# Optimization experiments

Measured on AMD Instinct MI355X. Metric: run time of the kernel, lower is better.

Reference implementation:

```python
import jax, jax.numpy as jnp
import numpy as np

N_HEADS = 16
KV_HEADS = 4
HEAD_DIM = 128
D_MODEL = N_HEADS * HEAD_DIM  # 2048
KV_DIM = KV_HEADS * HEAD_DIM  # 512
MAX_POS = 4096
ROPE_THETA = 10000.0
EPS = 1e-5


def _rope_cache(seq_len):
    # QEffMolmoRotaryEmbedding: inv_freq over head_dim, emb = cat(freqs, freqs)
    inv_freq = 1.0 / (ROPE_THETA ** (jnp.arange(0, HEAD_DIM, 2, dtype=jnp.float32) / HEAD_DIM))
    t = jnp.arange(seq_len, dtype=jnp.float32)
    freqs = jnp.outer(t, inv_freq)                      # [S, D/2]
    emb = jnp.concatenate([freqs, freqs], axis=-1)      # [S, D]
    return jnp.cos(emb), jnp.sin(emb)


def _rotate_half(x):
    # x: [B, H, T, D] -> cat(-x2, x1) with halves along last dim
    x1, x2 = jnp.split(x, 2, axis=-1)
    return jnp.concatenate([-x2, x1], axis=-1)


def _rms_norm(x, w):
    var = jnp.mean(jnp.square(x), axis=-1, keepdims=True)
    return (x * jax.lax.rsqrt(var + EPS)) * w


def setup_inputs() -> dict:
    key = jax.random.key(0)
    ks = jax.random.split(key, 8)
    B, T = 1, 2048
    q = jax.random.normal(ks[0], (B, T, D_MODEL), dtype=jnp.float32)
    k = jax.random.normal(ks[1], (B, T, KV_DIM), dtype=jnp.float32)
    v = jax.random.normal(ks[2], (B, T, KV_DIM), dtype=jnp.float32)
    # causal mask: True means masked (torch.where(mask, -10000, scores))
    attention_mask = jnp.triu(jnp.ones((T, T), dtype=bool), k=1)[None, None]  # [1,1,T,T]
    position_ids = jnp.arange(T, dtype=jnp.int32)[None, :]                    # [B,T]
    q_norm_w = jax.random.normal(ks[3], (D_MODEL,), dtype=jnp.float32) * 0.02 + 1.0
    k_norm_w = jax.random.normal(ks[4], (KV_DIM,), dtype=jnp.float32) * 0.02 + 1.0
    w_out = jax.random.normal(ks[5], (D_MODEL, D_MODEL), dtype=jnp.float32) * (D_MODEL ** -0.5)
    return {"q": q, "k": k, "v": v, "attention_mask": attention_mask,
            "position_ids": position_ids, "q_norm_w": q_norm_w,
            "k_norm_w": k_norm_w, "w_out": w_out}


def reference(q, k, v, attention_mask, position_ids, q_norm_w, k_norm_w, w_out):
    B, T, C = q.shape
    # QK-norm on flat projections
    q = _rms_norm(q, q_norm_w)
    k = _rms_norm(k, k_norm_w)
    # split heads: [B, H, T, D]
    q = q.reshape(B, T, N_HEADS, HEAD_DIM).transpose(0, 2, 1, 3)
    k = k.reshape(B, T, KV_HEADS, HEAD_DIM).transpose(0, 2, 1, 3)
    v = v.reshape(B, T, KV_HEADS, HEAD_DIM).transpose(0, 2, 1, 3)
    # RoPE (rotate_half variant)
    cos_c, sin_c = _rope_cache(MAX_POS)
    cos = cos_c[position_ids][:, None]  # [B,1,T,D]
    sin = sin_c[position_ids][:, None]
    q = q * cos + _rotate_half(q) * sin
    k = k * cos + _rotate_half(k) * sin
    # GQA expand
    rep = N_HEADS // KV_HEADS
    k = jnp.repeat(k, rep, axis=1)
    v = jnp.repeat(v, rep, axis=1)
    scale = 1.0 / np.sqrt(HEAD_DIM)
    scores = jnp.einsum('bhqd,bhkd->bhqk', q, k) * scale  # [B,H,T,T]
    scores = jnp.where(attention_mask, jnp.float32(-10000.0), scores)
    attn = jax.nn.softmax(scores.astype(jnp.float32), axis=-1).astype(q.dtype)
    out = jnp.einsum('bhqk,bhkd->bhqd', attn, v)          # [B,H,T,D]
    out = out.transpose(0, 2, 1, 3).reshape(B, T, C)
    return out @ w_out.T
```

## Files before the change

kernel.cpp:

```cpp
#include <hip/hip_runtime.h>
#include <hip/hip_bf16.h>
#include <math.h>

#define T_SEQ 2048
#define NH 16
#define KVH 4
#define HD 128
#define DM 2048
#define KVD 512

typedef short bf16x8 __attribute__((ext_vector_type(8)));
typedef float f32x4 __attribute__((ext_vector_type(4)));
typedef float f32x16 __attribute__((ext_vector_type(16)));
typedef unsigned int uint2v __attribute__((ext_vector_type(2)));

static __device__ __forceinline__ unsigned short f2bf(float f) {
    unsigned int x = __float_as_uint(f);
    x += 0x7fff + ((x >> 16) & 1);
    return (unsigned short)(x >> 16);
}
static __device__ __forceinline__ float bf2f(unsigned short u) {
    return __uint_as_float(((unsigned int)u) << 16);
}

static __device__ __forceinline__ unsigned int cvtpk(float lo, float hi) {
    unsigned int r;
    asm("v_cvt_pk_bf16_f32 %0, %1, %2" : "=v"(r) : "v"(lo), "v"(hi));
    return r;
}

static __device__ __forceinline__ f32x4 mfma16(bf16x8 a, bf16x8 b, f32x4 c) {
    return __builtin_amdgcn_mfma_f32_16x16x32_bf16(a, b, c, 0, 0, 0);
}
static __device__ __forceinline__ f32x16 mfma32(bf16x8 a, bf16x8 b, f32x16 c) {
    return __builtin_amdgcn_mfma_f32_32x32x16_bf16(a, b, c, 0, 0, 0);
}

static __device__ __forceinline__ void gl_lds16(const unsigned short* g, unsigned short* l) {
    __builtin_amdgcn_global_load_lds(
        (const __attribute__((address_space(1))) unsigned int*)g,
        (__attribute__((address_space(3))) unsigned int*)l,
        16, 0, 0);
}


__global__ __launch_bounds__(256) void prep_all(
    const float* __restrict__ q, const float* __restrict__ k,
    const float* __restrict__ qw, const float* __restrict__ kw,
    const int* __restrict__ pos_ids,
    unsigned short* __restrict__ Qb, unsigned short* __restrict__ Ks,
    const float* __restrict__ v, unsigned short* __restrict__ Vs,
    const float* __restrict__ w, unsigned short* __restrict__ Wf) {
    int bid = blockIdx.x;
    int tid = threadIdx.x;
    __shared__ float smem[DM + KVD + 64 + 64 + 8];

    if (bid < 2048) {
        float* qr = smem;
        float* kr = smem + DM;
        float* cosL = smem + DM + KVD;
        float* sinL = cosL + 64;
        float* redq = sinL + 64;
        float* redk = redq + 4;
        int t = bid;
        float qs = 0.f, ks = 0.f;
        {
            const float* qp = q + (size_t)t * DM + tid * 8;
            float4 v0 = *(const float4*)(qp);
            float4 v1 = *(const float4*)(qp + 4);
            float* dst = qr + tid * 8;
            dst[0] = v0.x; dst[1] = v0.y; dst[2] = v0.z; dst[3] = v0.w;
            dst[4] = v1.x; dst[5] = v1.y; dst[6] = v1.z; dst[7] = v1.w;
            qs = v0.x * v0.x + v0.y * v0.y + v0.z * v0.z + v0.w * v0.w +
                 v1.x * v1.x + v1.y * v1.y + v1.z * v1.z + v1.w * v1.w;
            float2 kv = *(const float2*)(k + (size_t)t * KVD + tid * 2);
            kr[tid * 2] = kv.x; kr[tid * 2 + 1] = kv.y;
            ks = kv.x * kv.x + kv.y * kv.y;
        }
        if (tid < 64) {
            float pos = (float)pos_ids[t];
            float inv = powf(10000.0f, -(float)tid * (1.0f / 64.0f));
            float a = pos * inv;
            cosL[tid] = cosf(a);
            sinL[tid] = sinf(a);
        }
        for (int off = 32; off; off >>= 1) {
            qs += __shfl_down(qs, off);
            ks += __shfl_down(ks, off);
        }
        if ((tid & 63) == 0) { redq[tid >> 6] = qs; redk[tid >> 6] = ks; }
        __syncthreads();
        float qinv = rsqrtf((redq[0] + redq[1] + redq[2] + redq[3]) * (1.0f / DM) + 1e-5f);
        float kinv = rsqrtf((redk[0] + redk[1] + redk[2] + redk[3]) * (1.0f / KVD) + 1e-5f);
        {
            int base = tid * 8;
            int h = base >> 7;
            int d = base & 127;
            bool lo = d < 64;
            int i0 = d & 63;
            int pb = lo ? base + 64 : base - 64;
            #pragma unroll
            for (int j = 0; j < 8; ++j) {
                float xv = qr[base + j] * qinv * qw[base + j];
                float pv = qr[pb + j] * qinv * qw[pb + j];
                float c = cosL[i0 + j];
                float s = sinL[i0 + j];
                float o = lo ? (xv * c - pv * s) : (xv * c + pv * s);
                Qb[((size_t)h * T_SEQ + t) * HD + d + j] = f2bf(o);
            }
        }
        {
            int base = tid * 2;
            int kh = base >> 7;
            int d = base & 127;
            bool lo = d < 64;
            int i0 = d & 63;
            int pb = lo ? base + 64 : base - 64;
            int kt = t >> 5, lq = t & 31;
            #pragma unroll
            for (int j = 0; j < 2; ++j) {
                float xv = kr[base + j] * kinv * kw[base + j];
                float pv = kr[pb + j] * kinv * kw[pb + j];
                float c = cosL[i0 + j];
                float s = sinL[i0 + j];
                float o = lo ? (xv * c - pv * s) : (xv * c + pv * s);
                int dj = d + j;
                int sl = dj >> 4, hi2 = (dj >> 3) & 1, jj = dj & 7;
                size_t oi = ((((size_t)(kh * 64 + kt) * 8 + sl) * 2 + hi2) * 32 + lq) * 8 + jj;
                Ks[oi] = f2bf(o);
            }
        }
        return;
    }
    if (bid < 2304) {
        unsigned short* tile = (unsigned short*)smem;
        int vb = bid - 2048;
        int tb = vb & 31;
        int cb = vb >> 5;
        #pragma unroll 4
        for (int rep = 0; rep < 16; ++rep) {
            int e = rep * 256 + tid;
            int r = e >> 6;
            int c = e & 63;
            tile[c * 80 + r] = f2bf(v[(size_t)(tb * 64 + r) * KVD + cb * 64 + c]);
        }
        __syncthreads();
        #pragma unroll
        for (int rep = 0; rep < 2; ++rep) {
            int e = rep * 256 + tid;
            int cc = e >> 3, tg = e & 7;
            int cg = cb * 64 + cc;
            int kh = cg >> 7, crow = cg & 127, db = crow >> 5, lq = crow & 31;
            int t0g = tb * 64 + tg * 8;
            int kt = t0g >> 5, tr = t0g & 31, half = tr >> 4, hi2 = (tr >> 3) & 1;
            size_t o = (((((size_t)(kh * 64 + kt) * 2 + half) * 4 + db) * 2 + hi2) * 32 + lq) * 8;
            *(bf16x8*)(Vs + o) = *(const bf16x8*)(&tile[cc * 80 + tg * 8]);
        }
        return;
    }
    {
        size_t idx = ((size_t)(bid - 2304) * 256 + tid) * 4;
        int row = (int)(idx >> 11);
        int col = (int)(idx & 2047);
        float4 f = *(const float4*)(w + idx);
        ushort4 o;
        o.x = f2bf(f.x); o.y = f2bf(f.y); o.z = f2bf(f.z); o.w = f2bf(f.w);
        int nt = row >> 6, wn2 = (row >> 5) & 1, jb = (row >> 4) & 1, lr = row & 15;
        int kt = col >> 6, ks = (col >> 5) & 1, hi2 = (col >> 3) & 3, jj = col & 7;
        size_t off = (((size_t)(nt * 32 + kt) * 8) + (wn2 * 2 + jb) * 2 + ks) * 512
                   + (lr + 16 * hi2) * 8 + jj;
        *(ushort4*)(Wf + off) = o;
    }
}

#define BEXP 20.0f
#define SCALE2 (0.08838834764831845f * 1.4426950408889634f)

#define STAGE1(B, S, KT)                                                           \
    do {                                                                           \
        const unsigned short* kg_ = Kt_g + (size_t)(KT) * 4096;                    \
        const unsigned short* vg_ = Vt_g + (size_t)(KT) * 4096;                    \
        gl_lds16(kg_ + w * 512 + l * 8,        &kv[B][S][w * 512]);                \
        gl_lds16(kg_ + 2048 + w * 512 + l * 8, &kv[B][S][2048 + w * 512]);         \
        gl_lds16(vg_ + w * 512 + l * 8,        &kv[B][S][4096 + w * 512]);         \
        gl_lds16(vg_ + 2048 + w * 512 + l * 8, &kv[B][S][6144 + w * 512]);         \
    } while (0)

#define TILE_COMPUTE(BUF, SLOT, KT)                                                \
    do {                                                                           \
        const unsigned short* kl = &kv[BUF][SLOT][0] + l * 8;                      \
        const unsigned short* vl = &kv[BUF][SLOT][4096] + l * 8;                   \
        f32x16 sa, sb;                                                             \
        _Pragma("unroll") for (int r = 0; r < 16; ++r) { sa[r] = 0.f; sb[r] = 0.f; } \
        __builtin_amdgcn_s_setprio(1);                                             \
        _Pragma("unroll") for (int x = 0; x < 8; x += 2) {                         \
            bf16x8 k0 = *(const bf16x8*)(kl + x * 512);                            \
            bf16x8 k1 = *(const bf16x8*)(kl + (x + 1) * 512);                      \
            sa = mfma32(k0, qf[x], sa);                                            \
            sb = mfma32(k1, qf[x + 1], sb);                                        \
        }                                                                          \
        __builtin_amdgcn_s_setprio(0);                                             \
        float p_[16];                                                              \
        if ((KT) == nkt - 1) {                                                     \
            int lim = qglob - (KT) * 32;                                           \
            _Pragma("unroll") for (int r = 0; r < 16; ++r) {                       \
                float e_ = __builtin_amdgcn_exp2f((sa[r] + sb[r]) * SCALE2 - BEXP); \
                int off_ = (r & 3) + 8 * (r >> 2) + 4 * hi;                        \
                p_[r] = (off_ <= lim) ? e_ : 0.f;                                  \
                sden4[r & 3] += p_[r];                                             \
            }                                                                      \
        } else {                                                                   \
            _Pragma("unroll") for (int r = 0; r < 16; ++r) {                       \
                p_[r] = __builtin_amdgcn_exp2f((sa[r] + sb[r]) * SCALE2 - BEXP);   \
                sden4[r & 3] += p_[r];                                             \
            }                                                                      \
        }                                                                          \
        __builtin_amdgcn_s_setprio(1);                                             \
        _Pragma("unroll") for (int half = 0; half < 2; ++half) {                   \
            unsigned int a0 = cvtpk(p_[half * 8 + 0], p_[half * 8 + 1]);           \
            unsigned int a1 = cvtpk(p_[half * 8 + 2], p_[half * 8 + 3]);           \
            unsigned int b0 = cvtpk(p_[half * 8 + 4], p_[half * 8 + 5]);           \
            unsigned int b1 = cvtpk(p_[half * 8 + 6], p_[half * 8 + 7]);           \
            uint2v w0 = __builtin_amdgcn_permlane32_swap(a0, b0, false, false);    \
            uint2v w1 = __builtin_amdgcn_permlane32_swap(a1, b1, false, false);    \
            union { unsigned int u[4]; bf16x8 v; } pc;                             \
            pc.u[0] = w0[0]; pc.u[1] = w1[0]; pc.u[2] = w0[1]; pc.u[3] = w1[1];    \
            bf16x8 pf = pc.v;                                                      \
            _Pragma("unroll") for (int db = 0; db < 4; ++db) {                     \
                bf16x8 vf = *(const bf16x8*)(vl + (half * 4 + db) * 512);          \
                oacc[db] = mfma32(vf, pf, oacc[db]);                               \
            }                                                                      \
        }                                                                          \
        __builtin_amdgcn_s_setprio(0);                                             \
    } while (0)

__global__ __launch_bounds__(256) void attn_fwd22(
    const unsigned short* __restrict__ Qb, const unsigned short* __restrict__ Ks,
    const unsigned short* __restrict__ Vs,
    unsigned short* __restrict__ Opart, float* __restrict__ Lpart,
    unsigned short* __restrict__ Xf, int CHUNK) {
    int fid = blockIdx.x;
    int sid = fid >> 2;
    int kh = fid & 3;
    int qrow, seg;
    if (sid < 60)       { qrow = 63 - sid / 3;          seg = sid % 3; }
    else if (sid < 104) { int t2 = sid - 60; qrow = 43 - (t2 >> 1); seg = t2 & 1; }
    else                { qrow = 21 - (sid - 104);      seg = 0; }

    int tid = threadIdx.x;
    int w = tid >> 6, l = tid & 63;
    int h = kh * 4 + w;
    int lq = l & 31, hi = l >> 5;
    int qglob = qrow * 32 + lq;

    int nkt = qrow + 1;
    int t0 = seg * CHUNK;
    int t1 = min(t0 + CHUNK, nkt);
    size_t idx = (size_t)(h * 64 + qrow) * 4 + seg;

    const unsigned short* Qh = Qb + (size_t)h * T_SEQ * HD;
    const unsigned short* Kt_g = Ks + (size_t)kh * 64 * 4096;
    const unsigned short* Vt_g = Vs + (size_t)kh * 64 * 4096;

    __shared__ unsigned short kv[2][2][8192];

    bf16x8 qf[8];
    #pragma unroll
    for (int sl = 0; sl < 8; ++sl)
        qf[sl] = *(const bf16x8*)(Qh + (size_t)qglob * HD + sl * 16 + hi * 8);

    f32x16 oacc[4];
    #pragma unroll
    for (int db = 0; db < 4; ++db)
        #pragma unroll
        for (int r = 0; r < 16; ++r) oacc[db][r] = 0.f;
    f32x4 sden4 = (f32x4){0.f, 0.f, 0.f, 0.f};

    int pairsEnd = t0 + ((t1 - t0) & ~1);
    int kt = t0;
    int cur = 0;
    if (kt < pairsEnd) { STAGE1(0, 0, kt); STAGE1(0, 1, kt + 1); }
    if (kt + 2 < pairsEnd) { STAGE1(1, 0, kt + 2); STAGE1(1, 1, kt + 3); }
    for (; kt < pairsEnd; kt += 2) {
        bool more = (kt + 2 < pairsEnd);
        if (more) asm volatile("s_waitcnt vmcnt(8)" ::: "memory");
        else      asm volatile("s_waitcnt vmcnt(0)" ::: "memory");
        __builtin_amdgcn_s_barrier();
        TILE_COMPUTE(cur, 0, kt);
        TILE_COMPUTE(cur, 1, kt + 1);
        asm volatile("s_waitcnt lgkmcnt(0)" ::: "memory");
        __builtin_amdgcn_s_barrier();
        if (kt + 4 < pairsEnd) { STAGE1(cur, 0, kt + 4); STAGE1(cur, 1, kt + 5); }
        cur ^= 1;
    }
    if (kt < t1) {
        STAGE1(cur, 0, kt);
        asm volatile("s_waitcnt vmcnt(0)" ::: "memory");
        __builtin_amdgcn_s_barrier();
        TILE_COMPUTE(cur, 0, kt);
    }

    float sden = (sden4[0] + sden4[1]) + (sden4[2] + sden4[3]);
    float sden_tot = sden + __shfl_xor(sden, 32);

    if (t0 == 0 && t1 == nkt) {
        float invs = 1.0f / sden_tot;
        int mt = qglob >> 7, wmrow = (qglob >> 6) & 1, ii = (qglob >> 4) & 3, lr = qglob & 15;
        size_t baseA = (((size_t)mt * 32) * 16 + (wmrow * 4 + ii) * 2) * 512 + lr * 8;
        #pragma unroll
        for (int db = 0; db < 4; ++db) {
            size_t bdb = baseA + (size_t)(h * 2 + (db >> 1)) * 8192 + (size_t)(db & 1) * 512;
            #pragma unroll
            for (int r = 0; r < 16; ++r) {
                size_t off = bdb + (r >> 2) * 128 + (r & 3) + 4 * hi;
                Xf[off] = f2bf(oacc[db][r] * invs);
            }
        }
        return;
    }
    if (hi == 0) Lpart[idx * 32 + lq] = sden_tot;
    unsigned short* op = Opart + (idx << 12);
    #pragma unroll
    for (int db = 0; db < 4; ++db) {
        #pragma unroll
        for (int r = 0; r < 16; ++r) {
            int d = db * 32 + (r & 3) + 8 * (r >> 2) + 4 * hi;
            op[d * 32 + lq] = f2bf(oacc[db][r]);
        }
    }
}

__global__ __launch_bounds__(256) void attn_combine(
    const unsigned short* __restrict__ Opart, const float* __restrict__ Lpart,
    unsigned short* __restrict__ Xf, int CHUNK) {
    int qrow = CHUNK + blockIdx.x;
    int h = blockIdx.y;
    int tid = threadIdx.x;
    int nkt = qrow + 1;
    int used = (nkt + CHUNK - 1) / CHUNK;
    int base = (h * 64 + qrow) * 4;
    __shared__ float invden[32];
    if (tid < 32) {
        int q = tid;
        float den = 0.f;
        for (int s = 0; s < used; ++s) den += Lpart[(base + s) * 32 + q];
        invden[q] = 1.0f / den;
    }
    __syncthreads();
    int d = tid >> 1, q0 = (tid & 1) * 16;
    float acc[16];
    #pragma unroll
    for (int j = 0; j < 16; ++j) acc[j] = 0.f;
    for (int s = 0; s < used; ++s) {
        const unsigned short* op = Opart + ((size_t)(base + s) << 12) + d * 32 + q0;
        bf16x8 o0 = *(const bf16x8*)(op);
        bf16x8 o1 = *(const bf16x8*)(op + 8);
        #pragma unroll
        for (int j = 0; j < 8; ++j) {
            acc[j]     += bf2f((unsigned short)o0[j]);
            acc[8 + j] += bf2f((unsigned short)o1[j]);
        }
    }
    __shared__ unsigned short xo[32][136];
    #pragma unroll
    for (int j = 0; j < 16; ++j)
        xo[q0 + j][d] = f2bf(acc[j] * invden[q0 + j]);
    __syncthreads();
    int q = tid >> 3, dc = (tid & 7) * 16;
    bf16x8 v0 = *(const bf16x8*)(&xo[q][dc]);
    bf16x8 v1 = *(const bf16x8*)(&xo[q][dc + 8]);
    int row = qrow * 32 + q;
    int mt = row >> 7, wmrow = (row >> 6) & 1, ii = (row >> 4) & 3, lr = row & 15;
    int kt = h * 2 + (dc >> 6);
    int ks = (dc >> 5) & 1;
    int hi2 = (dc >> 3) & 3;
    size_t off = (((size_t)(mt * 32 + kt) * 16) + (wmrow * 4 + ii) * 2 + ks) * 512
               + (lr + 16 * hi2) * 8;
    *(bf16x8*)(Xf + off) = v0;
    *(bf16x8*)(Xf + off + 128) = v1;
}

__global__ __launch_bounds__(256) void outproj3(
    const unsigned short* __restrict__ Xf, const unsigned short* __restrict__ Wf,
    float* __restrict__ out) {
    __shared__ unsigned short Af[2][8192];
    __shared__ unsigned short Bf[2][4096];
    int tid = threadIdx.x;
    int w = tid >> 6, l = tid & 63;
    int lr = l & 15, lg = l >> 4;
    int wm = w >> 1, wn = w & 1;
    int id = blockIdx.x;
    int wg = (id & 7) * 64 + (id >> 3);
    int s = wg >> 5, wi = wg & 31;
    int mb = (s & 3) * 4 + (wi & 3);
    int nb = (s >> 2) * 8 + (wi >> 2);
    int m0 = mb * 128, n0 = nb * 64;

    const unsigned short* Xt = Xf + ((size_t)mb * 32 * 16) * 512 + l * 8;
    const unsigned short* Wt = Wf + ((size_t)nb * 32 * 8) * 512 + l * 8;

    f32x4 acc[4][2];
    #pragma unroll
    for (int i = 0; i < 4; ++i)
        #pragma unroll
        for (int j = 0; j < 2; ++j) acc[i][j] = (f32x4){0.f, 0.f, 0.f, 0.f};

#define OSTAGE(B, KT)                                                              \
    do {                                                                           \
        const unsigned short* xa = Xt + (size_t)(KT) * 8192;                       \
        const unsigned short* wb_ = Wt + (size_t)(KT) * 4096;                      \
        _Pragma("unroll") for (int u = 0; u < 4; ++u)                              \
            gl_lds16(xa + (w * 4 + u) * 512, &Af[B][(w * 4 + u) * 512]);           \
        _Pragma("unroll") for (int u = 0; u < 2; ++u)                              \
            gl_lds16(wb_ + (w * 2 + u) * 512, &Bf[B][(w * 2 + u) * 512]);          \
    } while (0)

    OSTAGE(0, 0);
    OSTAGE(1, 1);
    int cur = 0;
    for (int t = 0; t < 32; ++t) {
        if (t + 1 < 32) asm volatile("s_waitcnt vmcnt(6)" ::: "memory");
        else            asm volatile("s_waitcnt vmcnt(0)" ::: "memory");
        __builtin_amdgcn_s_barrier();
        __builtin_amdgcn_s_setprio(1);
        #pragma unroll
        for (int ks = 0; ks < 2; ++ks) {
            bf16x8 af[4], bfr[2];
            #pragma unroll
            for (int i = 0; i < 4; ++i)
                af[i] = *(const bf16x8*)(&Af[cur][((wm * 4 + i) * 2 + ks) * 512] + l * 8);
            #pragma unroll
            for (int j = 0; j < 2; ++j)
                bfr[j] = *(const bf16x8*)(&Bf[cur][((wn * 2 + j) * 2 + ks) * 512] + l * 8);
            #pragma unroll
            for (int i = 0; i < 4; ++i)
                #pragma unroll
                for (int j = 0; j < 2; ++j)
                    acc[i][j] = mfma16(af[i], bfr[j], acc[i][j]);
        }
        __builtin_amdgcn_s_setprio(0);
        asm volatile("s_waitcnt lgkmcnt(0)" ::: "memory");
        __builtin_amdgcn_s_barrier();
        if (t + 2 < 32) OSTAGE(cur, t + 2);
        cur ^= 1;
    }
    #pragma unroll
    for (int i = 0; i < 4; ++i) {
        #pragma unroll
        for (int j = 0; j < 2; ++j) {
            #pragma unroll
            for (int r = 0; r < 4; ++r) {
                int row = m0 + wm * 64 + i * 16 + lg * 4 + r;
                int col = n0 + wn * 32 + j * 16 + lr;
                out[(size_t)row * DM + col] = acc[i][j][r];
            }
        }
    }
}

extern "C" void kernel_launch(void* const* d_in, const int* in_sizes, int n_in,
                              void* d_out, int out_size, void* d_ws, size_t ws_size,
                              hipStream_t stream) {
    const float* q = (const float*)d_in[0];
    const float* k = (const float*)d_in[1];
    const float* v = (const float*)d_in[2];
    const int* pos_ids = (const int*)d_in[4];
    const float* qw = (const float*)d_in[5];
    const float* kw = (const float*)d_in[6];
    const float* wout = (const float*)d_in[7];
    float* out = (float*)d_out;

    char* ws = (char*)d_ws;
    unsigned short* Qb = (unsigned short*)(ws + 0x100000);
    unsigned short* Ks = (unsigned short*)(ws + 0x900000);
    unsigned short* Vs = (unsigned short*)(ws + 0xB00000);
    unsigned short* Wf = (unsigned short*)(ws + 0xD00000);
    unsigned short* Xf = (unsigned short*)(ws + 0x1500000);
    float* Lpart = (float*)(ws + 0x1D00000);
    unsigned short* Opart = (unsigned short*)(ws + 0x1E00000);

    int CHUNK = (ws_size >= 0x1E00000ull + 4ull * 0x800000ull) ? 22 : 64;

    prep_all<<<2048 + 256 + 4096, 256, 0, stream>>>(q, k, qw, kw, pos_ids, Qb, Ks,
                                                    v, Vs, wout, Wf);
    if (CHUNK == 22) {
        attn_fwd22<<<504, 256, 0, stream>>>(Qb, Ks, Vs, Opart, Lpart, Xf, CHUNK);
        attn_combine<<<dim3(64 - 22, NH), 256, 0, stream>>>(Opart, Lpart, Xf, CHUNK);
    } else {
        attn_fwd22<<<504, 256, 0, stream>>>(Qb, Ks, Vs, Opart, Lpart, Xf, 64);
    }
    outproj3<<<512, 256, 0, stream>>>(Xf, Wf, out);
}
```

Baseline: 85.23 us.

## Enlarge output-projection tile to 128x128 with 512-thread blocks

The output projection GEMM now uses 128x128 output tiles computed by 8 waves in a 512-thread block, instead of 128x64 tiles with 4 waves. Grid size halves to 256 blocks, and the block-to-tile mapping and LDS staging of the weight tile are rearranged so each wave loads two A and two B subtiles. The aim is to raise reuse of the activation tile and cut global/L2 traffic per FLOP. The cost is twice the LDS per block and fewer blocks than CUs on a 256-CU part, which may reduce occupancy and latency hiding.

```diff
diff --git a/kernel.cpp b/kernel.cpp
--- a/kernel.cpp
+++ b/kernel.cpp
@@ -380,24 +380,26 @@
     *(bf16x8*)(Xf + off + 128) = v1;
 }
 
-__global__ __launch_bounds__(256) void outproj3(
+__global__ __launch_bounds__(512) void outproj4(
     const unsigned short* __restrict__ Xf, const unsigned short* __restrict__ Wf,
     float* __restrict__ out) {
     __shared__ unsigned short Af[2][8192];
-    __shared__ unsigned short Bf[2][4096];
+    __shared__ unsigned short Bf[2][8192];
     int tid = threadIdx.x;
     int w = tid >> 6, l = tid & 63;
     int lr = l & 15, lg = l >> 4;
-    int wm = w >> 1, wn = w & 1;
+    int wm = w >> 2, wn = w & 3;
     int id = blockIdx.x;
-    int wg = (id & 7) * 64 + (id >> 3);
-    int s = wg >> 5, wi = wg & 31;
-    int mb = (s & 3) * 4 + (wi & 3);
-    int nb = (s >> 2) * 8 + (wi >> 2);
-    int m0 = mb * 128, n0 = nb * 64;
+    int wg = (id & 7) * 32 + (id >> 3);
+    int mb = wg >> 4, nb = wg & 15;
+    int m0 = mb * 128, n0 = nb * 128;
 
     const unsigned short* Xt = Xf + ((size_t)mb * 32 * 16) * 512 + l * 8;
-    const unsigned short* Wt = Wf + ((size_t)nb * 32 * 8) * 512 + l * 8;
+    const unsigned short* Wp = Wf + ((size_t)(nb * 2 + (w >> 2)) * 32 * 8) * 512 + l * 8;
+    int aw = w * 2;
+    int bw = (w & 3) * 2;
+    unsigned short* BfBase0 = &Bf[0][(w >> 2) * 4096];
+    unsigned short* BfBase1 = &Bf[1][(w >> 2) * 4096];
 
     f32x4 acc[4][2];
     #pragma unroll
@@ -405,21 +407,22 @@
         #pragma unroll
         for (int j = 0; j < 2; ++j) acc[i][j] = (f32x4){0.f, 0.f, 0.f, 0.f};
 
-#define OSTAGE(B, KT)                                                              \
+#define OSTG(B, KT)                                                                \
     do {                                                                           \
         const unsigned short* xa = Xt + (size_t)(KT) * 8192;                       \
-        const unsigned short* wb_ = Wt + (size_t)(KT) * 4096;                      \
-        _Pragma("unroll") for (int u = 0; u < 4; ++u)                              \
-            gl_lds16(xa + (w * 4 + u) * 512, &Af[B][(w * 4 + u) * 512]);           \
-        _Pragma("unroll") for (int u = 0; u < 2; ++u)                              \
-            gl_lds16(wb_ + (w * 2 + u) * 512, &Bf[B][(w * 2 + u) * 512]);          \
+        const unsigned short* wa = Wp + (size_t)(KT) * 4096;                       \
+        gl_lds16(xa + aw * 512,       &Af[B][aw * 512]);                           \
+        gl_lds16(xa + (aw + 1) * 512, &Af[B][(aw + 1) * 512]);                     \
+        unsigned short* bb = (B) ? BfBase1 : BfBase0;                              \
+        gl_lds16(wa + bw * 512,       bb + bw * 512);                              \
+        gl_lds16(wa + (bw + 1) * 512, bb + (bw + 1) * 512);                        \
     } while (0)
 
-    OSTAGE(0, 0);
-    OSTAGE(1, 1);
+    OSTG(0, 0);
+    OSTG(1, 1);
     int cur = 0;
     for (int t = 0; t < 32; ++t) {
-        if (t + 1 < 32) asm volatile("s_waitcnt vmcnt(6)" ::: "memory");
+        if (t + 1 < 32) asm volatile("s_waitcnt vmcnt(4)" ::: "memory");
         else            asm volatile("s_waitcnt vmcnt(0)" ::: "memory");
         __builtin_amdgcn_s_barrier();
         __builtin_amdgcn_s_setprio(1);
@@ -431,7 +434,8 @@
                 af[i] = *(const bf16x8*)(&Af[cur][((wm * 4 + i) * 2 + ks) * 512] + l * 8);
             #pragma unroll
             for (int j = 0; j < 2; ++j)
-                bfr[j] = *(const bf16x8*)(&Bf[cur][((wn * 2 + j) * 2 + ks) * 512] + l * 8);
+                bfr[j] = *(const bf16x8*)(&Bf[cur][(wn >> 1) * 4096 +
+                                                   (((wn & 1) * 2 + j) * 2 + ks) * 512] + l * 8);
             #pragma unroll
             for (int i = 0; i < 4; ++i)
                 #pragma unroll
@@ -441,7 +445,7 @@
         __builtin_amdgcn_s_setprio(0);
         asm volatile("s_waitcnt lgkmcnt(0)" ::: "memory");
         __builtin_amdgcn_s_barrier();
-        if (t + 2 < 32) OSTAGE(cur, t + 2);
+        if (t + 2 < 32) OSTG(cur, t + 2);
         cur ^= 1;
     }
     #pragma unroll
@@ -489,5 +493,5 @@
     } else {
         attn_fwd22<<<504, 256, 0, stream>>>(Qb, Ks, Vs, Opart, Lpart, Xf, 64);
     }
-    outproj3<<<512, 256, 0, stream>>>(Xf, Wf, out);
-}
+    outproj4<<<256, 512, 0, stream>>>(Xf, Wf, out);
+}
```

Result: slower. 89.64 us (+5.2%).
